# Kernel tuning notes

Hardware: AMD Instinct MI355X
Metric: run time of the kernel (lower is better)

## Reference

```python
import jax, jax.numpy as jnp
import numpy as np

FEATURE_TO_DENSE_SCALE = 64.0
DENSE_TO_DENSE_SCALE = 64.0
OUTPUT_SCALE = 16.0
TOTAL_FEATURES = 81920
HIDDEN = 512
L1 = 32
L2 = 32
B = 8192
NNZ = 32


def setup_inputs() -> dict:
    key = jax.random.key(0)
    ks = jax.random.split(key, 12)
    white_idx = jax.random.randint(ks[0], (B, NNZ), 0, TOTAL_FEATURES, dtype=jnp.int64 if jax.config.jax_enable_x64 else jnp.int32)
    black_idx = jax.random.randint(ks[1], (B, NNZ), 0, TOTAL_FEATURES, dtype=white_idx.dtype)
    # make a few indices -1 to exercise the invalid-index mask path
    mask_w = jax.random.uniform(ks[2], (B, NNZ)) < 0.05
    mask_b = jax.random.uniform(ks[3], (B, NNZ)) < 0.05
    white_idx = jnp.where(mask_w, -1, white_idx)
    black_idx = jnp.where(mask_b, -1, black_idx)
    stm = jax.random.randint(ks[4], (B,), 0, 2, dtype=white_idx.dtype)
    white_vals = jax.random.uniform(ks[5], (B, NNZ), dtype=jnp.float32)
    black_vals = jax.random.uniform(ks[6], (B, NNZ), dtype=jnp.float32)
    ft_weight = jax.random.normal(ks[7], (TOTAL_FEATURES, HIDDEN), dtype=jnp.float32) * 0.02
    ft_bias = jnp.zeros((HIDDEN,), dtype=jnp.float32)
    d1_w = jax.random.normal(ks[8], (L1, HIDDEN), dtype=jnp.float32) * (1.0 / np.sqrt(HIDDEN))
    d1_b = jnp.zeros((L1,), dtype=jnp.float32)
    d2_w = jax.random.normal(ks[9], (L2, L1), dtype=jnp.float32) * (1.0 / np.sqrt(L1))
    d2_b = jnp.zeros((L2,), dtype=jnp.float32)
    out_w = jax.random.normal(ks[10], (1, L2), dtype=jnp.float32) * (1.0 / np.sqrt(L2))
    out_b = jnp.zeros((1,), dtype=jnp.float32)
    return dict(white_idx=white_idx, black_idx=black_idx, stm=stm,
                white_vals=white_vals, black_vals=black_vals,
                ft_weight=ft_weight, ft_bias=ft_bias,
                d1_w=d1_w, d1_b=d1_b, d2_w=d2_w, d2_b=d2_b,
                out_w=out_w, out_b=out_b)


def _feature_transform(weight, bias, indices, values):
    # indices: [B, NNZ]; weight: [F, H]
    valid = (indices >= 0)
    safe = jnp.maximum(indices, 0)
    gathered = weight[safe]                         # [B, NNZ, H]
    scale = values * valid.astype(values.dtype)     # fuse value scale + mask
    acc = jnp.einsum('bnh,bn->bh', gathered, scale) # gather-scale-reduce
    return acc + bias


def reference(white_idx, black_idx, stm, white_vals, black_vals,
              ft_weight, ft_bias, d1_w, d1_b, d2_w, d2_b, out_w, out_b):
    white_acc = _feature_transform(ft_weight, ft_bias, white_idx, white_vals)
    black_acc = _feature_transform(ft_weight, ft_bias, black_idx, black_vals)
    white_stm = (stm == 0)[:, None]
    us = jnp.where(white_stm, white_acc, black_acc)
    them = jnp.where(white_stm, black_acc, white_acc)
    x = jax.nn.relu((us - them) / FEATURE_TO_DENSE_SCALE)
    x = jax.nn.relu((x @ d1_w.T + d1_b) / DENSE_TO_DENSE_SCALE)
    x = jax.nn.relu((x @ d2_w.T + d2_b) / DENSE_TO_DENSE_SCALE)
    x = (x @ out_w.T + out_b)[:, 0] / OUTPUT_SCALE
    return x
```

## Files before the change

kernel.cpp:

```cpp
#include <hip/hip_runtime.h>

#define NNZ 32
#define HIDDEN 512

__global__ __launch_bounds__(256) void cvt_bf16(const uint4* __restrict__ in,
                                                uint2* __restrict__ out, int n4)
{
    const int i = blockIdx.x * 256 + threadIdx.x;
    if (i >= n4) return;
    uint4 v = in[i];
    #define CV(u) (((u) + 0x7FFFu + (((u) >> 16) & 1u)) >> 16)
    uint2 o;
    o.x = CV(v.x) | (CV(v.y) << 16);
    o.y = CV(v.z) | (CV(v.w) << 16);
    #undef CV
    out[i] = o;
}

__global__ __launch_bounds__(256, 5) void nnue_wave(
    const int* __restrict__ white_idx, const int* __restrict__ black_idx,
    const int* __restrict__ stm,
    const float* __restrict__ white_vals, const float* __restrict__ black_vals,
    const uint4* __restrict__ Wq,
    const uint2* __restrict__ W1b,
    const float* __restrict__ d1_b,
    const float* __restrict__ d2_w, const float* __restrict__ d2_b,
    const float* __restrict__ out_w, const float* __restrict__ out_b,
    float* __restrict__ out, int B)
{
    const int lane = threadIdx.x & 63;
    const int wv   = threadIdx.x >> 6;
    const int b    = (blockIdx.x << 2) | wv;
    if (b >= B) return;

    __shared__ float xbuf[4][HIDDEN];
    __shared__ float h1buf[4][32];

    int   id;
    float val;
    {
        const int  n = lane & 31;
        const bool w = lane < 32;
        const int*   ip = w ? white_idx  : black_idx;
        const float* vp = w ? white_vals : black_vals;
        id  = ip[b * NNZ + n];
        val = vp[b * NNZ + n];
        if (id < 0) { id = 0; val = 0.f; }
    }

    float accW[8], accB[8];
    #pragma unroll
    for (int j = 0; j < 8; ++j) { accW[j] = 0.f; accB[j] = 0.f; }

    #define FT_BATCH(RB, ACC)                                                         \
    {                                                                                 \
        uint4 w[8]; float vv[8];                                                      \
        _Pragma("unroll")                                                             \
        for (int u = 0; u < 8; ++u) {                                                 \
            const int sid = __builtin_amdgcn_readlane(id, (RB) + u);                  \
            vv[u] = __uint_as_float(                                                  \
                (unsigned)__builtin_amdgcn_readlane(__float_as_int(val), (RB) + u));  \
            w[u] = Wq[(size_t)sid * 64 + lane];                                       \
        }                                                                             \
        _Pragma("unroll")                                                             \
        for (int u = 0; u < 8; ++u) {                                                 \
            const unsigned* pw = (const unsigned*)&w[u];                              \
            _Pragma("unroll")                                                         \
            for (int j = 0; j < 4; ++j) {                                             \
                ACC[2*j]   = fmaf(vv[u], __uint_as_float(pw[j] << 16),         ACC[2*j]);   \
                ACC[2*j+1] = fmaf(vv[u], __uint_as_float(pw[j] & 0xFFFF0000u), ACC[2*j+1]); \
            }                                                                         \
        }                                                                             \
    }

    FT_BATCH(0,  accW) FT_BATCH(8,  accW) FT_BATCH(16, accW) FT_BATCH(24, accW)
    FT_BATCH(32, accB) FT_BATCH(40, accB) FT_BATCH(48, accB) FT_BATCH(56, accB)
    #undef FT_BATCH

    const float sgn   = (stm[b] == 0) ? 1.f : -1.f;
    const float inv64 = 0.015625f;
    float4 x0, x1;
    x0.x = fmaxf(sgn * (accW[0] - accB[0]) * inv64, 0.f);
    x0.y = fmaxf(sgn * (accW[1] - accB[1]) * inv64, 0.f);
    x0.z = fmaxf(sgn * (accW[2] - accB[2]) * inv64, 0.f);
    x0.w = fmaxf(sgn * (accW[3] - accB[3]) * inv64, 0.f);
    x1.x = fmaxf(sgn * (accW[4] - accB[4]) * inv64, 0.f);
    x1.y = fmaxf(sgn * (accW[5] - accB[5]) * inv64, 0.f);
    x1.z = fmaxf(sgn * (accW[6] - accB[6]) * inv64, 0.f);
    x1.w = fmaxf(sgn * (accW[7] - accB[7]) * inv64, 0.f);
    *(float4*)&xbuf[wv][lane * 8]     = x0;
    *(float4*)&xbuf[wv][lane * 8 + 4] = x1;

    const int o = lane >> 1, h = lane & 1;
    const uint2* w1p = W1b + o * 128 + h * 64;
    const float* xh  = &xbuf[wv][h * 256];
    float p = 0.f;
    #pragma unroll 8
    for (int kk = 0; kk < 64; ++kk) {
        const uint2  ww = w1p[kk];
        const float4 xv = *(const float4*)&xh[kk * 4];
        p = fmaf(xv.x, __uint_as_float(ww.x << 16),         p);
        p = fmaf(xv.y, __uint_as_float(ww.x & 0xFFFF0000u), p);
        p = fmaf(xv.z, __uint_as_float(ww.y << 16),         p);
        p = fmaf(xv.w, __uint_as_float(ww.y & 0xFFFF0000u), p);
    }
    p += __shfl_xor(p, 1);
    if (h == 0) h1buf[wv][o] = fmaxf((p + d1_b[o]) * inv64, 0.f);

    const int o2 = lane & 31;
    const float* w2p = d2_w + o2 * 32;
    float q = d2_b[o2];
    #pragma unroll
    for (int k = 0; k < 32; ++k) q = fmaf(h1buf[wv][k], w2p[k], q);
    const float h2 = fmaxf(q * inv64, 0.f);

    float t = h2 * out_w[o2];
    #pragma unroll
    for (int s = 1; s < 32; s <<= 1) t += __shfl_xor(t, s);
    if (lane == 0) out[b] = (t + out_b[0]) * 0.0625f;
}

__global__ __launch_bounds__(256) void nnue_fused_f32(
    const int* __restrict__ white_idx, const int* __restrict__ black_idx,
    const int* __restrict__ stm,
    const float* __restrict__ white_vals, const float* __restrict__ black_vals,
    const float* __restrict__ ft_weight,
    const float* __restrict__ d1_w, const float* __restrict__ d1_b,
    const float* __restrict__ d2_w, const float* __restrict__ d2_b,
    const float* __restrict__ out_w, const float* __restrict__ out_b,
    float* __restrict__ out)
{
    const int b   = blockIdx.x;
    const int tid = threadIdx.x;

    __shared__ int   s_idx[64];
    __shared__ float s_val[64];
    __shared__ float s_accB[HIDDEN];
    __shared__ float xs[HIDDEN];
    __shared__ float part[32][9];
    __shared__ float h1s[32];
    __shared__ float h2s[32];

    if (tid < 64) {
        const int sd = tid >> 5;
        const int n  = tid & 31;
        const int*   ip = sd ? black_idx  : white_idx;
        const float* vp = sd ? black_vals : white_vals;
        int   id = ip[b * NNZ + n];
        float v  = vp[b * NNZ + n];
        if (id < 0) { id = 0; v = 0.f; }
        s_idx[tid] = id;
        s_val[tid] = v;
    }
    __syncthreads();

    const int side = tid >> 7;
    const int lane = tid & 127;
    const int base = side << 5;

    const float4* W = reinterpret_cast<const float4*>(ft_weight);
    float4 acc = make_float4(0.f, 0.f, 0.f, 0.f);
    #pragma unroll
    for (int c = 0; c < NNZ; c += 8) {
        float4 w[8];
        float  vv[8];
        #pragma unroll
        for (int u = 0; u < 8; ++u) {
            const int n = base + c + u;
            w[u]  = W[(size_t)s_idx[n] * (HIDDEN / 4) + lane];
            vv[u] = s_val[n];
        }
        #pragma unroll
        for (int u = 0; u < 8; ++u) {
            acc.x = fmaf(vv[u], w[u].x, acc.x);
            acc.y = fmaf(vv[u], w[u].y, acc.y);
            acc.z = fmaf(vv[u], w[u].z, acc.z);
            acc.w = fmaf(vv[u], w[u].w, acc.w);
        }
    }

    if (side == 1) reinterpret_cast<float4*>(s_accB)[lane] = acc;
    __syncthreads();
    if (side == 0) {
        const float4 aB  = reinterpret_cast<const float4*>(s_accB)[lane];
        const float sgn  = (stm[b] == 0) ? 1.f : -1.f;
        const float inv64 = 1.0f / 64.0f;
        float4 x;
        x.x = fmaxf(sgn * (acc.x - aB.x) * inv64, 0.f);
        x.y = fmaxf(sgn * (acc.y - aB.y) * inv64, 0.f);
        x.z = fmaxf(sgn * (acc.z - aB.z) * inv64, 0.f);
        x.w = fmaxf(sgn * (acc.w - aB.w) * inv64, 0.f);
        reinterpret_cast<float4*>(xs)[lane] = x;
    }
    __syncthreads();
    {
        const int o = tid & 31;
        const int j = tid >> 5;
        const float* w1p = d1_w + o * HIDDEN + j * 64;
        const float* xp  = xs + j * 64;
        float p = 0.f;
        #pragma unroll
        for (int k = 0; k < 64; ++k) p = fmaf(xp[k], w1p[k], p);
        part[o][j] = p;
    }
    __syncthreads();
    if (tid < 32) {
        const float inv64 = 1.0f / 64.0f;
        float s = d1_b[tid];
        #pragma unroll
        for (int j = 0; j < 8; ++j) s += part[tid][j];
        h1s[tid] = fmaxf(s * inv64, 0.f);
    }
    __syncthreads();
    if (tid < 32) {
        const float inv64 = 1.0f / 64.0f;
        const float* w2p = d2_w + tid * 32;
        float s = d2_b[tid];
        #pragma unroll
        for (int k = 0; k < 32; ++k) s = fmaf(h1s[k], w2p[k], s);
        h2s[tid] = fmaxf(s * inv64, 0.f);
    }
    __syncthreads();
    if (tid == 0) {
        float s = out_b[0];
        #pragma unroll
        for (int k = 0; k < 32; ++k) s = fmaf(h2s[k], out_w[k], s);
        out[b] = s * (1.0f / 16.0f);
    }
}

extern "C" void kernel_launch(void* const* d_in, const int* in_sizes, int n_in,
                              void* d_out, int out_size, void* d_ws, size_t ws_size,
                              hipStream_t stream) {
    const int*   white_idx  = (const int*)d_in[0];
    const int*   black_idx  = (const int*)d_in[1];
    const int*   stm        = (const int*)d_in[2];
    const float* white_vals = (const float*)d_in[3];
    const float* black_vals = (const float*)d_in[4];
    const float* ft_weight  = (const float*)d_in[5];
    const float* d1_w       = (const float*)d_in[7];
    const float* d1_b       = (const float*)d_in[8];
    const float* d2_w       = (const float*)d_in[9];
    const float* d2_b       = (const float*)d_in[10];
    const float* out_w      = (const float*)d_in[11];
    const float* out_b      = (const float*)d_in[12];
    float*       out        = (float*)d_out;

    const int B  = in_sizes[2];
    const long long FH  = in_sizes[5];
    const long long W1N = in_sizes[7];

    if (ws_size >= (size_t)(FH * 2 + W1N * 2 + 256)) {
        const int n4  = (int)(FH / 4);
        const int n4w = (int)(W1N / 4);
        uint2* tblb = (uint2*)d_ws;
        uint2* w1b  = (uint2*)((char*)d_ws + (size_t)FH * 2);
        cvt_bf16<<<(n4 + 255) / 256, 256, 0, stream>>>((const uint4*)ft_weight, tblb, n4);
        cvt_bf16<<<(n4w + 255) / 256, 256, 0, stream>>>((const uint4*)d1_w, w1b, n4w);
        nnue_wave<<<(B + 3) / 4, 256, 0, stream>>>(white_idx, black_idx, stm,
                                                   white_vals, black_vals,
                                                   (const uint4*)tblb, (const uint2*)w1b,
                                                   d1_b, d2_w, d2_b,
                                                   out_w, out_b, out, B);
    } else {
        nnue_fused_f32<<<B, 256, 0, stream>>>(white_idx, black_idx, stm,
                                              white_vals, black_vals,
                                              ft_weight,
                                              d1_w, d1_b, d2_w, d2_b,
                                              out_w, out_b, out);
    }
}
```

Baseline: 122.7 us.

## Overlap bf16 table conversion with fp32 processing of first samples

Merges the two bf16 conversion kernels into one launch and puts them in the same grid as an fp32 fused path that handles the first 1280 samples straight from the fp32 table. The remaining samples then run through the bf16 wave kernel. The aim is to hide the conversion pass behind useful work and save launch overhead. In exchange, the first samples use the slower fp32 gather path, the workspace size check is gone, and the two block types compete for bandwidth.

```diff
diff --git a/kernel.cpp b/kernel.cpp
--- a/kernel.cpp
+++ b/kernel.cpp
@@ -3,18 +3,139 @@
 #define NNZ 32
 #define HIDDEN 512
 
-__global__ __launch_bounds__(256) void cvt_bf16(const uint4* __restrict__ in,
-                                                uint2* __restrict__ out, int n4)
-{
-    const int i = blockIdx.x * 256 + threadIdx.x;
-    if (i >= n4) return;
-    uint4 v = in[i];
+__device__ __forceinline__ uint2 cvt4_bf16(uint4 v) {
     #define CV(u) (((u) + 0x7FFFu + (((u) >> 16) & 1u)) >> 16)
     uint2 o;
     o.x = CV(v.x) | (CV(v.y) << 16);
     o.y = CV(v.z) | (CV(v.w) << 16);
     #undef CV
-    out[i] = o;
+    return o;
+}
+
+__global__ __launch_bounds__(256) void nnue_phase1(
+    const int* __restrict__ white_idx, const int* __restrict__ black_idx,
+    const int* __restrict__ stm,
+    const float* __restrict__ white_vals, const float* __restrict__ black_vals,
+    const float* __restrict__ ft_weight,
+    const float* __restrict__ d1_w, const float* __restrict__ d1_b,
+    const float* __restrict__ d2_w, const float* __restrict__ d2_b,
+    const float* __restrict__ out_w, const float* __restrict__ out_b,
+    float* __restrict__ out,
+    uint2* __restrict__ tblb, uint2* __restrict__ w1b,
+    int GB, int nCvtBlocks, int n4, int n4w)
+{
+    const int bid = blockIdx.x;
+    const int tid = threadIdx.x;
+
+    if (bid >= GB) {
+        if (bid < GB + 16) {
+            const int i = (bid - GB) * 256 + tid;
+            if (i < n4w)
+                w1b[i] = cvt4_bf16(reinterpret_cast<const uint4*>(d1_w)[i]);
+        } else {
+            const int stride = nCvtBlocks * 256;
+            for (int i = (bid - GB - 16) * 256 + tid; i < n4; i += stride)
+                tblb[i] = cvt4_bf16(reinterpret_cast<const uint4*>(ft_weight)[i]);
+        }
+        return;
+    }
+
+    const int b = bid;
+
+    __shared__ int   s_idx[64];
+    __shared__ float s_val[64];
+    __shared__ float s_accB[HIDDEN];
+    __shared__ float xs[HIDDEN];
+    __shared__ float part[32][9];
+    __shared__ float h1s[32];
+    __shared__ float h2s[32];
+
+    if (tid < 64) {
+        const int sd = tid >> 5;
+        const int n  = tid & 31;
+        const int*   ip = sd ? black_idx  : white_idx;
+        const float* vp = sd ? black_vals : white_vals;
+        int   id = ip[b * NNZ + n];
+        float v  = vp[b * NNZ + n];
+        if (id < 0) { id = 0; v = 0.f; }
+        s_idx[tid] = id;
+        s_val[tid] = v;
+    }
+    __syncthreads();
+
+    const int side = tid >> 7;
+    const int lane = tid & 127;
+    const int base = side << 5;
+
+    const float4* W = reinterpret_cast<const float4*>(ft_weight);
+    float4 acc = make_float4(0.f, 0.f, 0.f, 0.f);
+    #pragma unroll
+    for (int c = 0; c < NNZ; c += 8) {
+        float4 w[8];
+        float  vv[8];
+        #pragma unroll
+        for (int u = 0; u < 8; ++u) {
+            const int n = base + c + u;
+            w[u]  = W[(size_t)s_idx[n] * (HIDDEN / 4) + lane];
+            vv[u] = s_val[n];
+        }
+        #pragma unroll
+        for (int u = 0; u < 8; ++u) {
+            acc.x = fmaf(vv[u], w[u].x, acc.x);
+            acc.y = fmaf(vv[u], w[u].y, acc.y);
+            acc.z = fmaf(vv[u], w[u].z, acc.z);
+            acc.w = fmaf(vv[u], w[u].w, acc.w);
+        }
+    }
+
+    if (side == 1) reinterpret_cast<float4*>(s_accB)[lane] = acc;
+    __syncthreads();
+    if (side == 0) {
+        const float4 aB  = reinterpret_cast<const float4*>(s_accB)[lane];
+        const float sgn  = (stm[b] == 0) ? 1.f : -1.f;
+        const float inv64 = 1.0f / 64.0f;
+        float4 x;
+        x.x = fmaxf(sgn * (acc.x - aB.x) * inv64, 0.f);
+        x.y = fmaxf(sgn * (acc.y - aB.y) * inv64, 0.f);
+        x.z = fmaxf(sgn * (acc.z - aB.z) * inv64, 0.f);
+        x.w = fmaxf(sgn * (acc.w - aB.w) * inv64, 0.f);
+        reinterpret_cast<float4*>(xs)[lane] = x;
+    }
+    __syncthreads();
+    {
+        const int o = tid & 31;
+        const int j = tid >> 5;
+        const float* w1p = d1_w + o * HIDDEN + j * 64;
+        const float* xp  = xs + j * 64;
+        float p = 0.f;
+        #pragma unroll
+        for (int k = 0; k < 64; ++k) p = fmaf(xp[k], w1p[k], p);
+        part[o][j] = p;
+    }
+    __syncthreads();
+    if (tid < 32) {
+        const float inv64 = 1.0f / 64.0f;
+        float s = d1_b[tid];
+        #pragma unroll
+        for (int j = 0; j < 8; ++j) s += part[tid][j];
+        h1s[tid] = fmaxf(s * inv64, 0.f);
+    }
+    __syncthreads();
+    if (tid < 32) {
+        const float inv64 = 1.0f / 64.0f;
+        const float* w2p = d2_w + tid * 32;
+        float s = d2_b[tid];
+        #pragma unroll
+        for (int k = 0; k < 32; ++k) s = fmaf(h1s[k], w2p[k], s);
+        h2s[tid] = fmaxf(s * inv64, 0.f);
+    }
+    __syncthreads();
+    if (tid == 0) {
+        float s = out_b[0];
+        #pragma unroll
+        for (int k = 0; k < 32; ++k) s = fmaf(h2s[k], out_w[k], s);
+        out[b] = s * (1.0f / 16.0f);
+    }
 }
 
 __global__ __launch_bounds__(256, 5) void nnue_wave(
@@ -26,11 +147,11 @@
     const float* __restrict__ d1_b,
     const float* __restrict__ d2_w, const float* __restrict__ d2_b,
     const float* __restrict__ out_w, const float* __restrict__ out_b,
-    float* __restrict__ out, int B)
+    float* __restrict__ out, int sample0, int B)
 {
     const int lane = threadIdx.x & 63;
     const int wv   = threadIdx.x >> 6;
-    const int b    = (blockIdx.x << 2) | wv;
+    const int b    = sample0 + ((blockIdx.x << 2) | wv);
     if (b >= B) return;
 
     __shared__ float xbuf[4][HIDDEN];
@@ -120,115 +241,6 @@
     if (lane == 0) out[b] = (t + out_b[0]) * 0.0625f;
 }
 
-__global__ __launch_bounds__(256) void nnue_fused_f32(
-    const int* __restrict__ white_idx, const int* __restrict__ black_idx,
-    const int* __restrict__ stm,
-    const float* __restrict__ white_vals, const float* __restrict__ black_vals,
-    const float* __restrict__ ft_weight,
-    const float* __restrict__ d1_w, const float* __restrict__ d1_b,
-    const float* __restrict__ d2_w, const float* __restrict__ d2_b,
-    const float* __restrict__ out_w, const float* __restrict__ out_b,
-    float* __restrict__ out)
-{
-    const int b   = blockIdx.x;
-    const int tid = threadIdx.x;
-
-    __shared__ int   s_idx[64];
-    __shared__ float s_val[64];
-    __shared__ float s_accB[HIDDEN];
-    __shared__ float xs[HIDDEN];
-    __shared__ float part[32][9];
-    __shared__ float h1s[32];
-    __shared__ float h2s[32];
-
-    if (tid < 64) {
-        const int sd = tid >> 5;
-        const int n  = tid & 31;
-        const int*   ip = sd ? black_idx  : white_idx;
-        const float* vp = sd ? black_vals : white_vals;
-        int   id = ip[b * NNZ + n];
-        float v  = vp[b * NNZ + n];
-        if (id < 0) { id = 0; v = 0.f; }
-        s_idx[tid] = id;
-        s_val[tid] = v;
-    }
-    __syncthreads();
-
-    const int side = tid >> 7;
-    const int lane = tid & 127;
-    const int base = side << 5;
-
-    const float4* W = reinterpret_cast<const float4*>(ft_weight);
-    float4 acc = make_float4(0.f, 0.f, 0.f, 0.f);
-    #pragma unroll
-    for (int c = 0; c < NNZ; c += 8) {
-        float4 w[8];
-        float  vv[8];
-        #pragma unroll
-        for (int u = 0; u < 8; ++u) {
-            const int n = base + c + u;
-            w[u]  = W[(size_t)s_idx[n] * (HIDDEN / 4) + lane];
-            vv[u] = s_val[n];
-        }
-        #pragma unroll
-        for (int u = 0; u < 8; ++u) {
-            acc.x = fmaf(vv[u], w[u].x, acc.x);
-            acc.y = fmaf(vv[u], w[u].y, acc.y);
-            acc.z = fmaf(vv[u], w[u].z, acc.z);
-            acc.w = fmaf(vv[u], w[u].w, acc.w);
-        }
-    }
-
-    if (side == 1) reinterpret_cast<float4*>(s_accB)[lane] = acc;
-    __syncthreads();
-    if (side == 0) {
-        const float4 aB  = reinterpret_cast<const float4*>(s_accB)[lane];
-        const float sgn  = (stm[b] == 0) ? 1.f : -1.f;
-        const float inv64 = 1.0f / 64.0f;
-        float4 x;
-        x.x = fmaxf(sgn * (acc.x - aB.x) * inv64, 0.f);
-        x.y = fmaxf(sgn * (acc.y - aB.y) * inv64, 0.f);
-        x.z = fmaxf(sgn * (acc.z - aB.z) * inv64, 0.f);
-        x.w = fmaxf(sgn * (acc.w - aB.w) * inv64, 0.f);
-        reinterpret_cast<float4*>(xs)[lane] = x;
-    }
-    __syncthreads();
-    {
-        const int o = tid & 31;
-        const int j = tid >> 5;
-        const float* w1p = d1_w + o * HIDDEN + j * 64;
-        const float* xp  = xs + j * 64;
-        float p = 0.f;
-        #pragma unroll
-        for (int k = 0; k < 64; ++k) p = fmaf(xp[k], w1p[k], p);
-        part[o][j] = p;
-    }
-    __syncthreads();
-    if (tid < 32) {
-        const float inv64 = 1.0f / 64.0f;
-        float s = d1_b[tid];
-        #pragma unroll
-        for (int j = 0; j < 8; ++j) s += part[tid][j];
-        h1s[tid] = fmaxf(s * inv64, 0.f);
-    }
-    __syncthreads();
-    if (tid < 32) {
-        const float inv64 = 1.0f / 64.0f;
-        const float* w2p = d2_w + tid * 32;
-        float s = d2_b[tid];
-        #pragma unroll
-        for (int k = 0; k < 32; ++k) s = fmaf(h1s[k], w2p[k], s);
-        h2s[tid] = fmaxf(s * inv64, 0.f);
-    }
-    __syncthreads();
-    if (tid == 0) {
-        float s = out_b[0];
-        #pragma unroll
-        for (int k = 0; k < 32; ++k) s = fmaf(h2s[k], out_w[k], s);
-        out[b] = s * (1.0f / 16.0f);
-    }
-}
-
 extern "C" void kernel_launch(void* const* d_in, const int* in_sizes, int n_in,
                               void* d_out, int out_size, void* d_ws, size_t ws_size,
                               hipStream_t stream) {
@@ -250,23 +262,26 @@
     const long long FH  = in_sizes[5];
     const long long W1N = in_sizes[7];
 
-    if (ws_size >= (size_t)(FH * 2 + W1N * 2 + 256)) {
-        const int n4  = (int)(FH / 4);
-        const int n4w = (int)(W1N / 4);
-        uint2* tblb = (uint2*)d_ws;
-        uint2* w1b  = (uint2*)((char*)d_ws + (size_t)FH * 2);
-        cvt_bf16<<<(n4 + 255) / 256, 256, 0, stream>>>((const uint4*)ft_weight, tblb, n4);
-        cvt_bf16<<<(n4w + 255) / 256, 256, 0, stream>>>((const uint4*)d1_w, w1b, n4w);
-        nnue_wave<<<(B + 3) / 4, 256, 0, stream>>>(white_idx, black_idx, stm,
-                                                   white_vals, black_vals,
-                                                   (const uint4*)tblb, (const uint2*)w1b,
-                                                   d1_b, d2_w, d2_b,
-                                                   out_w, out_b, out, B);
-    } else {
-        nnue_fused_f32<<<B, 256, 0, stream>>>(white_idx, black_idx, stm,
-                                              white_vals, black_vals,
-                                              ft_weight,
-                                              d1_w, d1_b, d2_w, d2_b,
-                                              out_w, out_b, out);
-    }
-}
+    uint2* tblb = (uint2*)d_ws;
+    uint2* w1b  = (uint2*)((char*)d_ws + (size_t)FH * 2);
+
+    const int n4  = (int)(FH / 4);
+    const int n4w = (int)(W1N / 4);
+
+    int C = 1280;
+    if (C > B) C = B & ~3;
+    const int nCvtBlocks = 1024;
+
+    nnue_phase1<<<C + 16 + nCvtBlocks, 256, 0, stream>>>(
+        white_idx, black_idx, stm, white_vals, black_vals,
+        ft_weight, d1_w, d1_b, d2_w, d2_b, out_w, out_b, out,
+        tblb, w1b, C, nCvtBlocks, n4, n4w);
+
+    const int rem = B - C;
+    if (rem > 0) {
+        nnue_wave<<<(rem + 3) / 4, 256, 0, stream>>>(
+            white_idx, black_idx, stm, white_vals, black_vals,
+            (const uint4*)tblb, (const uint2*)w1b,
+            d1_b, d2_w, d2_b, out_w, out_b, out, C, B);
+    }
+}
```

Result: slower. 138.0 us (+12.5%).
